# Kernel optimization log

Hardware: AMD Instinct MI355X
Metric: run time of the kernel (lower is better)

Reference implementation:

```python
import jax, jax.numpy as jnp
import numpy as np

NEG_BIG = -9e15  # matches torch's -9000000000000000.0 masked-fill value
ALPHA = 0.2      # LeakyReLU negative slope


def setup_inputs() -> dict:
    key = jax.random.key(0)
    k1, k2, k3, k4 = jax.random.split(key, 4)
    N, F_in, F_out = 8192, 128, 64
    h = jax.random.normal(k1, (N, F_in), dtype=jnp.float32)
    adj = jax.random.randint(k2, (N, N), 0, 2).astype(jnp.float32)
    # Glorot(gain=1.414)-scale params
    W = jax.random.normal(k3, (F_in, F_out), dtype=jnp.float32) * (1.414 * np.sqrt(2.0 / (F_in + F_out)))
    a = jax.random.normal(k4, (2 * F_out, 1), dtype=jnp.float32) * (1.414 * np.sqrt(2.0 / (2 * F_out + 1)))
    return {"h": h, "adj": adj, "W": W, "a": a}


def reference(h, adj, W, a):
    F_out = W.shape[1]
    Wh = h @ W                               # [N, F_out]
    Wh1 = Wh @ a[:F_out, :]                  # [N, 1]
    Wh2 = Wh @ a[F_out:, :]                  # [N, 1]
    e = jax.nn.leaky_relu(Wh1 + Wh2.T, negative_slope=ALPHA)  # [N, N]
    attention = jnp.where(adj > 0, e, NEG_BIG)
    attention = jax.nn.softmax(attention, axis=1)
    # dropout omitted (eval mode / p applied only in training)
    h_prime = attention @ Wh                 # [N, F_out]
    return jax.nn.elu(h_prime)               # concat=True -> ELU
```

## Files before the change

### kernel.cpp

```cpp
#include <hip/hip_runtime.h>
#include <hip/hip_bf16.h>

#define N 8192
#define FIN 128
#define FOUT 64
#define ALPHA 0.2f
#define LOG2E 1.44269504f
#define JSPLIT 4
#define JSPAN (N / JSPLIT)
#define STJ 256
#define NST (JSPAN / STJ)

typedef __attribute__((ext_vector_type(8))) short short8;
typedef __attribute__((ext_vector_type(4))) float f32x4;

static __device__ __forceinline__ unsigned fkey(float x) {
    unsigned u = __float_as_uint(x);
    return (u >> 31) ? ~u : (u | 0x80000000u);
}
static __device__ __forceinline__ float fdecode(unsigned k) {
    unsigned u = (k & 0x80000000u) ? (k & 0x7FFFFFFFu) : ~k;
    return __uint_as_float(u);
}
static __device__ __forceinline__ void gll16(const float* g, float* l) {
    __builtin_amdgcn_global_load_lds(
        (const __attribute__((address_space(1))) unsigned int*)g,
        (__attribute__((address_space(3))) unsigned int*)l, 16, 0, 0);
}

__global__ __launch_bounds__(256) void k_prep(const float* __restrict__ h,
                                              const float* __restrict__ W,
                                              const float* __restrict__ a,
                                              float* __restrict__ Wh,
                                              float* __restrict__ s2,
                                              float* __restrict__ t2,
                                              unsigned* __restrict__ keys) {
    __shared__ float lH[16 * FIN];
    __shared__ float lW[FIN * FOUT];
    __shared__ float red[8];
    const int tid = threadIdx.x;
    const int r0 = blockIdx.x * 16;
    {
        const float4* src = (const float4*)(h + (size_t)r0 * FIN);
        float4* dst = (float4*)lH;
        for (int i = tid; i < 16 * FIN / 4; i += 256) dst[i] = src[i];
        const float4* ws_ = (const float4*)W;
        float4* dw = (float4*)lW;
        for (int i = tid; i < FIN * FOUT / 4; i += 256) dw[i] = ws_[i];
    }
    __syncthreads();
    const int wave = tid >> 6, lane = tid & 63;
    float acc[4] = {0.f, 0.f, 0.f, 0.f};
    for (int k = 0; k < FIN; ++k) {
        float wv = lW[k * FOUT + lane];
#pragma unroll
        for (int r = 0; r < 4; ++r)
            acc[r] = fmaf(lH[(wave * 4 + r) * FIN + k], wv, acc[r]);
    }
    const float a1 = a[lane], a2 = a[FOUT + lane];
    float smx = -1e30f, tmx = -1e30f;
#pragma unroll
    for (int r = 0; r < 4; ++r) {
        int row = r0 + wave * 4 + r;
        Wh[(size_t)row * FOUT + lane] = acc[r];
        float sv = acc[r] * a1, tv = acc[r] * a2;
#pragma unroll
        for (int off = 32; off; off >>= 1) {
            sv += __shfl_xor(sv, off);
            tv += __shfl_xor(tv, off);
        }
        sv *= LOG2E; tv *= LOG2E;
        if (lane == 0) { s2[row] = sv; t2[row] = tv; }
        smx = fmaxf(smx, sv);
        tmx = fmaxf(tmx, tv);
    }
    if (lane == 0) { red[wave] = smx; red[4 + wave] = tmx; }
    __syncthreads();
    if (tid == 0) {
        float ms = fmaxf(fmaxf(red[0], red[1]), fmaxf(red[2], red[3]));
        float mt = fmaxf(fmaxf(red[4], red[5]), fmaxf(red[6], red[7]));
        atomicMax(keys + 0, fkey(ms));
        atomicMax(keys + 1, fkey(mt));
    }
}

__global__ __launch_bounds__(256) void k_pack(const float* __restrict__ Wh,
                                              __hip_bfloat16* __restrict__ WhB) {
    const int c = blockIdx.x;
    const int tn = threadIdx.x >> 6;
    const int lane = threadIdx.x & 63;
    const int quad = lane >> 4, l16 = lane & 15;
    const float* src = Wh + ((size_t)(c * 32 + quad * 8)) * FOUT + tn * 16 + l16;
    union { unsigned short u[8]; short8 v; } frag;
#pragma unroll
    for (int e = 0; e < 8; ++e) {
        __hip_bfloat16 b = __float2bfloat16(src[(size_t)e * FOUT]);
        frag.u[e] = *(unsigned short*)&b;
    }
    *(short8*)&WhB[(((size_t)c * 4 + tn) * 64 + lane) * 8] = frag.v;
}

__global__ __launch_bounds__(256) void k_attn(const float* __restrict__ adj,
                                              const __hip_bfloat16* __restrict__ WhB,
                                              const float* __restrict__ s2,
                                              const float* __restrict__ t2,
                                              const unsigned* __restrict__ keys,
                                              float* __restrict__ acc_ws,
                                              float* __restrict__ l_ws) {
    __shared__ float bufA[2][8 * 512];
    __shared__ float tl[JSPAN];
    const int wave = threadIdx.x >> 6, lane = threadIdx.x & 63;
    const int quad = lane >> 4, l16 = lane & 15;
    const int i0 = blockIdx.x * 16;
    const int jb = blockIdx.y * JSPAN;
    const int u0 = 2 * wave;

    {
        const float4* src = (const float4*)(t2 + jb);
        float4* dst = (float4*)tl;
        for (int i = threadIdx.x; i < JSPAN / 4; i += 256) dst[i] = src[i];
    }
    const float* gaw = adj + (size_t)(i0 + l16) * N + jb + quad * 8;
    gll16(gaw + u0 * 32,      &bufA[0][u0 * 512]);
    gll16(gaw + u0 * 32 + 4,  &bufA[0][u0 * 512 + 256]);
    gll16(gaw + u0 * 32 + 32, &bufA[0][(u0 + 1) * 512]);
    gll16(gaw + u0 * 32 + 36, &bufA[0][(u0 + 1) * 512 + 256]);

    const float mraw = fdecode(keys[0]) + fdecode(keys[1]);
    const float mm = mraw > 0.f ? mraw : ALPHA * mraw;
    const float sm = s2[i0 + l16];
    const short8* BF = (const short8*)WhB;

    f32x4 acc0 = {0,0,0,0}, acc1 = {0,0,0,0}, acc2 = {0,0,0,0}, acc3 = {0,0,0,0};
    float lsum = 0.f;
    __syncthreads();

    for (int st = 0; st < NST; ++st) {
        const int b = st & 1;
        const size_t kc = (size_t)(blockIdx.y * (JSPAN / 32) + st * 8 + u0) * 4;
        short8 B00 = BF[(kc + 0) * 64 + lane];
        short8 B01 = BF[(kc + 1) * 64 + lane];
        short8 B02 = BF[(kc + 2) * 64 + lane];
        short8 B03 = BF[(kc + 3) * 64 + lane];
        short8 B10 = BF[(kc + 4) * 64 + lane];
        short8 B11 = BF[(kc + 5) * 64 + lane];
        short8 B12 = BF[(kc + 6) * 64 + lane];
        short8 B13 = BF[(kc + 7) * 64 + lane];
        __builtin_amdgcn_sched_barrier(0);
        if (st + 1 < NST) {
            const float* g = gaw + (st + 1) * STJ + u0 * 32;
            float* d = &bufA[b ^ 1][u0 * 512];
            gll16(g, d);
            gll16(g + 4, d + 256);
            gll16(g + 32, d + 512);
            gll16(g + 36, d + 768);
        }
        __builtin_amdgcn_sched_barrier(0);
#pragma unroll
        for (int uu = 0; uu < 2; ++uu) {
            const int ul = u0 + uu;
            const float* Au = &bufA[b][ul * 512];
            float4 alo = *(const float4*)(Au + lane * 4);
            float4 ahi = *(const float4*)(Au + 256 + lane * 4);
            const float* Tp = tl + st * STJ + ul * 32 + quad * 8;
            float4 tlo = *(const float4*)Tp;
            float4 thi = *(const float4*)(Tp + 4);
            union { __hip_bfloat162 h2[4]; short8 v; } af;
#pragma unroll
            for (int pp = 0; pp < 4; ++pp) {
                float a0 = (pp < 2) ? ((const float*)&alo)[2 * pp]     : ((const float*)&ahi)[2 * pp - 4];
                float a1 = (pp < 2) ? ((const float*)&alo)[2 * pp + 1] : ((const float*)&ahi)[2 * pp - 3];
                float t0 = (pp < 2) ? ((const float*)&tlo)[2 * pp]     : ((const float*)&thi)[2 * pp - 4];
                float t1 = (pp < 2) ? ((const float*)&tlo)[2 * pp + 1] : ((const float*)&thi)[2 * pp - 3];
                float x0 = sm + t0,                x1 = sm + t1;
                float le0 = fmaxf(x0, ALPHA * x0), le1 = fmaxf(x1, ALPHA * x1);
                float p0 = a0 * exp2f(le0 - mm),   p1 = a1 * exp2f(le1 - mm);
                __hip_bfloat162 pb = __float22bfloat162_rn(make_float2(p0, p1));
                af.h2[pp] = pb;
                lsum += __bfloat162float(pb.x) + __bfloat162float(pb.y);
            }
            if (uu == 0) {
                acc0 = __builtin_amdgcn_mfma_f32_16x16x32_bf16(af.v, B00, acc0, 0, 0, 0);
                acc1 = __builtin_amdgcn_mfma_f32_16x16x32_bf16(af.v, B01, acc1, 0, 0, 0);
                acc2 = __builtin_amdgcn_mfma_f32_16x16x32_bf16(af.v, B02, acc2, 0, 0, 0);
                acc3 = __builtin_amdgcn_mfma_f32_16x16x32_bf16(af.v, B03, acc3, 0, 0, 0);
            } else {
                acc0 = __builtin_amdgcn_mfma_f32_16x16x32_bf16(af.v, B10, acc0, 0, 0, 0);
                acc1 = __builtin_amdgcn_mfma_f32_16x16x32_bf16(af.v, B11, acc1, 0, 0, 0);
                acc2 = __builtin_amdgcn_mfma_f32_16x16x32_bf16(af.v, B12, acc2, 0, 0, 0);
                acc3 = __builtin_amdgcn_mfma_f32_16x16x32_bf16(af.v, B13, acc3, 0, 0, 0);
            }
        }
        __syncthreads();
    }

    lsum += __shfl_xor(lsum, 16);
    lsum += __shfl_xor(lsum, 32);

    float* accr = &bufA[0][0];
    float* shlp = tl;
    *(f32x4*)&accr[((wave * 4 + 0) * 64 + lane) * 4] = acc0;
    *(f32x4*)&accr[((wave * 4 + 1) * 64 + lane) * 4] = acc1;
    *(f32x4*)&accr[((wave * 4 + 2) * 64 + lane) * 4] = acc2;
    *(f32x4*)&accr[((wave * 4 + 3) * 64 + lane) * 4] = acc3;
    if (lane < 16) shlp[wave * 16 + lane] = lsum;
    __syncthreads();

    const int tile = wave;
    f32x4 tot = {0, 0, 0, 0};
#pragma unroll
    for (int w = 0; w < 4; ++w) {
        f32x4 c = *(const f32x4*)&accr[((w * 4 + tile) * 64 + lane) * 4];
        tot[0] += c[0]; tot[1] += c[1]; tot[2] += c[2]; tot[3] += c[3];
    }
#pragma unroll
    for (int r = 0; r < 4; ++r) {
        int row = quad * 4 + r;
        atomicAdd(&acc_ws[(size_t)(i0 + row) * FOUT + tile * 16 + l16], tot[r]);
    }
    if (wave == 0 && lane < 16) {
        float lv = shlp[lane] + shlp[16 + lane] + shlp[32 + lane] + shlp[48 + lane];
        atomicAdd(&l_ws[i0 + lane], lv);
    }
}

__global__ __launch_bounds__(256) void k_final(const float* __restrict__ acc_ws,
                                               const float* __restrict__ l_ws,
                                               float* __restrict__ out) {
    const int idx = blockIdx.x * 256 + threadIdx.x;
    const int row = idx >> 4;
    const float inv = 1.0f / l_ws[row];
    float4 a = ((const float4*)acc_ws)[idx];
    float4 o;
#pragma unroll
    for (int r = 0; r < 4; ++r) {
        float v = ((const float*)&a)[r] * inv;
        ((float*)&o)[r] = v > 0.f ? v : (exp2f(v * LOG2E) - 1.f);
    }
    ((float4*)out)[idx] = o;
}

extern "C" void kernel_launch(void* const* d_in, const int* in_sizes, int n_in,
                              void* d_out, int out_size, void* d_ws, size_t ws_size,
                              hipStream_t stream) {
    const float* h   = (const float*)d_in[0];
    const float* adj = (const float*)d_in[1];
    const float* W   = (const float*)d_in[2];
    const float* a   = (const float*)d_in[3];
    float* out = (float*)d_out;

    char* base = (char*)d_ws;
    float* Wh = (float*)base;                        base += (size_t)N * FOUT * 4;
    __hip_bfloat16* WhB = (__hip_bfloat16*)base;     base += (size_t)N * FOUT * 2;
    float* s2 = (float*)base;                        base += (size_t)N * 4;
    float* t2 = (float*)base;                        base += (size_t)N * 4 + 1024;
    float* acc_ws = (float*)base;                    base += (size_t)N * FOUT * 4;
    float* l_ws = (float*)base;                      base += (size_t)N * 4;
    unsigned* keys = (unsigned*)base;

    hipMemsetAsync(acc_ws, 0, ((size_t)N * FOUT + N) * 4 + 2 * sizeof(unsigned), stream);
    k_prep<<<N / 16, 256, 0, stream>>>(h, W, a, Wh, s2, t2, keys);
    k_pack<<<N / 32, 256, 0, stream>>>(Wh, WhB);
    dim3 ag(N / 16, JSPLIT);
    k_attn<<<ag, 256, 0, stream>>>(adj, WhB, s2, t2, keys, acc_ws, l_ws);
    k_final<<<N * FOUT / 4 / 256, 256, 0, stream>>>(acc_ws, l_ws, out);
}
```

Baseline: 399.1 us.

## Restructure attention tile loads into row-contiguous, padded LDS with triple-stage prefetch

Each wave now loads four full adj rows with fully coalesced 16-byte-per-lane loads into padded LDS rows, instead of scattered 32-byte fragments. It computes the masked exponentials row-wise, writes bf16 probabilities to a separate padded LDS buffer, and reads them back in MFMA fragment layout. Prefetch now runs two stages ahead using manual waitcnt and raw s_barrier, and the row sums are reduced per row with shuffles. This targets better global-load coalescing and deeper memory latency hiding, at the cost of an extra LDS round trip and two barriers per stage. The reuse of buffer b for stage st+2 while other waves may still be reading it relies on the first barrier for ordering. The vmcnt handling inside the loop looks thin.

After: 407.6 us. 1.02x slower.

```diff
diff --git a/kernel.cpp b/kernel.cpp
--- a/kernel.cpp
+++ b/kernel.cpp
@@ -10,6 +10,8 @@
 #define JSPAN (N / JSPLIT)
 #define STJ 256
 #define NST (JSPAN / STJ)
+#define RSA 260
+#define RSP 264
 
 typedef __attribute__((ext_vector_type(8))) short short8;
 typedef __attribute__((ext_vector_type(4))) float f32x4;
@@ -107,37 +109,49 @@
                                               const unsigned* __restrict__ keys,
                                               float* __restrict__ acc_ws,
                                               float* __restrict__ l_ws) {
-    __shared__ float bufA[2][8 * 512];
+    __shared__ float bufA[2][16 * RSA];
+    __shared__ __hip_bfloat16 pbuf[16 * RSP];
     __shared__ float tl[JSPAN];
     const int wave = threadIdx.x >> 6, lane = threadIdx.x & 63;
     const int quad = lane >> 4, l16 = lane & 15;
     const int i0 = blockIdx.x * 16;
     const int jb = blockIdx.y * JSPAN;
-    const int u0 = 2 * wave;
-
-    {
-        const float4* src = (const float4*)(t2 + jb);
-        float4* dst = (float4*)tl;
-        for (int i = threadIdx.x; i < JSPAN / 4; i += 256) dst[i] = src[i];
-    }
-    const float* gaw = adj + (size_t)(i0 + l16) * N + jb + quad * 8;
-    gll16(gaw + u0 * 32,      &bufA[0][u0 * 512]);
-    gll16(gaw + u0 * 32 + 4,  &bufA[0][u0 * 512 + 256]);
-    gll16(gaw + u0 * 32 + 32, &bufA[0][(u0 + 1) * 512]);
-    gll16(gaw + u0 * 32 + 36, &bufA[0][(u0 + 1) * 512 + 256]);
+    const int r0 = 4 * wave;
+
+    for (int i = threadIdx.x; i < JSPAN / 4; i += 256)
+        ((float4*)tl)[i] = ((const float4*)(t2 + jb))[i];
+    asm volatile("s_waitcnt lgkmcnt(0)" ::: "memory");
+    __builtin_amdgcn_sched_barrier(0);
+
+    const float* g0 = adj + (size_t)(i0 + r0 + 0) * N + jb + lane * 4;
+    const float* g1 = g0 + N;
+    const float* g2 = g0 + 2 * N;
+    const float* g3 = g0 + 3 * N;
+
+    gll16(g0, &bufA[0][(r0 + 0) * RSA]);
+    gll16(g1, &bufA[0][(r0 + 1) * RSA]);
+    gll16(g2, &bufA[0][(r0 + 2) * RSA]);
+    gll16(g3, &bufA[0][(r0 + 3) * RSA]);
+    gll16(g0 + STJ, &bufA[1][(r0 + 0) * RSA]);
+    gll16(g1 + STJ, &bufA[1][(r0 + 1) * RSA]);
+    gll16(g2 + STJ, &bufA[1][(r0 + 2) * RSA]);
+    gll16(g3 + STJ, &bufA[1][(r0 + 3) * RSA]);
+    __builtin_amdgcn_sched_barrier(0);
+    asm volatile("s_waitcnt vmcnt(4)" ::: "memory");
 
     const float mraw = fdecode(keys[0]) + fdecode(keys[1]);
     const float mm = mraw > 0.f ? mraw : ALPHA * mraw;
-    const float sm = s2[i0 + l16];
+    float sr[4];
+#pragma unroll
+    for (int rr = 0; rr < 4; ++rr) sr[rr] = s2[i0 + r0 + rr];
     const short8* BF = (const short8*)WhB;
 
     f32x4 acc0 = {0,0,0,0}, acc1 = {0,0,0,0}, acc2 = {0,0,0,0}, acc3 = {0,0,0,0};
-    float lsum = 0.f;
-    __syncthreads();
+    float ls[4] = {0.f, 0.f, 0.f, 0.f};
 
     for (int st = 0; st < NST; ++st) {
         const int b = st & 1;
-        const size_t kc = (size_t)(blockIdx.y * (JSPAN / 32) + st * 8 + u0) * 4;
+        const size_t kc = ((size_t)blockIdx.y * (JSPAN / 32) + st * 8 + 2 * wave) * 4;
         short8 B00 = BF[(kc + 0) * 64 + lane];
         short8 B01 = BF[(kc + 1) * 64 + lane];
         short8 B02 = BF[(kc + 2) * 64 + lane];
@@ -147,65 +161,68 @@
         short8 B12 = BF[(kc + 6) * 64 + lane];
         short8 B13 = BF[(kc + 7) * 64 + lane];
         __builtin_amdgcn_sched_barrier(0);
-        if (st + 1 < NST) {
-            const float* g = gaw + (st + 1) * STJ + u0 * 32;
-            float* d = &bufA[b ^ 1][u0 * 512];
-            gll16(g, d);
-            gll16(g + 4, d + 256);
-            gll16(g + 32, d + 512);
-            gll16(g + 36, d + 768);
+        asm volatile("s_barrier" ::: "memory");
+        float4 tv = *(const float4*)&tl[st * STJ + lane * 4];
+#pragma unroll
+        for (int rr = 0; rr < 4; ++rr) {
+            float4 av = *(const float4*)&bufA[b][(r0 + rr) * RSA + lane * 4];
+            union { __hip_bfloat162 h2[2]; uint2 u2; } pk;
+            float lacc = 0.f;
+#pragma unroll
+            for (int pp = 0; pp < 2; ++pp) {
+                float x0 = sr[rr] + ((const float*)&tv)[2 * pp];
+                float x1 = sr[rr] + ((const float*)&tv)[2 * pp + 1];
+                float le0 = fmaxf(x0, ALPHA * x0), le1 = fmaxf(x1, ALPHA * x1);
+                float p0 = ((const float*)&av)[2 * pp] * exp2f(le0 - mm);
+                float p1 = ((const float*)&av)[2 * pp + 1] * exp2f(le1 - mm);
+                __hip_bfloat162 pb = __float22bfloat162_rn(make_float2(p0, p1));
+                pk.h2[pp] = pb;
+                lacc += __bfloat162float(pb.x) + __bfloat162float(pb.y);
+            }
+            *(uint2*)&pbuf[(r0 + rr) * RSP + lane * 4] = pk.u2;
+            ls[rr] += lacc;
         }
         __builtin_amdgcn_sched_barrier(0);
+        const int sd = (st + 2 < NST ? st + 2 : NST - 1) * STJ;
+        gll16(g0 + sd, &bufA[b][(r0 + 0) * RSA]);
+        gll16(g1 + sd, &bufA[b][(r0 + 1) * RSA]);
+        gll16(g2 + sd, &bufA[b][(r0 + 2) * RSA]);
+        gll16(g3 + sd, &bufA[b][(r0 + 3) * RSA]);
+        __builtin_amdgcn_sched_barrier(0);
+        asm volatile("s_waitcnt lgkmcnt(0)" ::: "memory");
+        asm volatile("s_barrier" ::: "memory");
 #pragma unroll
         for (int uu = 0; uu < 2; ++uu) {
-            const int ul = u0 + uu;
-            const float* Au = &bufA[b][ul * 512];
-            float4 alo = *(const float4*)(Au + lane * 4);
-            float4 ahi = *(const float4*)(Au + 256 + lane * 4);
-            const float* Tp = tl + st * STJ + ul * 32 + quad * 8;
-            float4 tlo = *(const float4*)Tp;
-            float4 thi = *(const float4*)(Tp + 4);
-            union { __hip_bfloat162 h2[4]; short8 v; } af;
-#pragma unroll
-            for (int pp = 0; pp < 4; ++pp) {
-                float a0 = (pp < 2) ? ((const float*)&alo)[2 * pp]     : ((const float*)&ahi)[2 * pp - 4];
-                float a1 = (pp < 2) ? ((const float*)&alo)[2 * pp + 1] : ((const float*)&ahi)[2 * pp - 3];
-                float t0 = (pp < 2) ? ((const float*)&tlo)[2 * pp]     : ((const float*)&thi)[2 * pp - 4];
-                float t1 = (pp < 2) ? ((const float*)&tlo)[2 * pp + 1] : ((const float*)&thi)[2 * pp - 3];
-                float x0 = sm + t0,                x1 = sm + t1;
-                float le0 = fmaxf(x0, ALPHA * x0), le1 = fmaxf(x1, ALPHA * x1);
-                float p0 = a0 * exp2f(le0 - mm),   p1 = a1 * exp2f(le1 - mm);
-                __hip_bfloat162 pb = __float22bfloat162_rn(make_float2(p0, p1));
-                af.h2[pp] = pb;
-                lsum += __bfloat162float(pb.x) + __bfloat162float(pb.y);
-            }
+            short8 af = *(const short8*)&pbuf[l16 * RSP + (2 * wave + uu) * 32 + quad * 8];
             if (uu == 0) {
-                acc0 = __builtin_amdgcn_mfma_f32_16x16x32_bf16(af.v, B00, acc0, 0, 0, 0);
-                acc1 = __builtin_amdgcn_mfma_f32_16x16x32_bf16(af.v, B01, acc1, 0, 0, 0);
-                acc2 = __builtin_amdgcn_mfma_f32_16x16x32_bf16(af.v, B02, acc2, 0, 0, 0);
-                acc3 = __builtin_amdgcn_mfma_f32_16x16x32_bf16(af.v, B03, acc3, 0, 0, 0);
+                acc0 = __builtin_amdgcn_mfma_f32_16x16x32_bf16(af, B00, acc0, 0, 0, 0);
+                acc1 = __builtin_amdgcn_mfma_f32_16x16x32_bf16(af, B01, acc1, 0, 0, 0);
+                acc2 = __builtin_amdgcn_mfma_f32_16x16x32_bf16(af, B02, acc2, 0, 0, 0);
+                acc3 = __builtin_amdgcn_mfma_f32_16x16x32_bf16(af, B03, acc3, 0, 0, 0);
             } else {
-                acc0 = __builtin_amdgcn_mfma_f32_16x16x32_bf16(af.v, B10, acc0, 0, 0, 0);
-                acc1 = __builtin_amdgcn_mfma_f32_16x16x32_bf16(af.v, B11, acc1, 0, 0, 0);
-                acc2 = __builtin_amdgcn_mfma_f32_16x16x32_bf16(af.v, B12, acc2, 0, 0, 0);
-                acc3 = __builtin_amdgcn_mfma_f32_16x16x32_bf16(af.v, B13, acc3, 0, 0, 0);
+                acc0 = __builtin_amdgcn_mfma_f32_16x16x32_bf16(af, B10, acc0, 0, 0, 0);
+                acc1 = __builtin_amdgcn_mfma_f32_16x16x32_bf16(af, B11, acc1, 0, 0, 0);
+                acc2 = __builtin_amdgcn_mfma_f32_16x16x32_bf16(af, B12, acc2, 0, 0, 0);
+                acc3 = __builtin_amdgcn_mfma_f32_16x16x32_bf16(af, B13, acc3, 0, 0, 0);
             }
         }
-        __syncthreads();
-    }
-
-    lsum += __shfl_xor(lsum, 16);
-    lsum += __shfl_xor(lsum, 32);
+    }
+    __syncthreads();
+
+#pragma unroll
+    for (int rr = 0; rr < 4; ++rr) {
+        float v = ls[rr];
+#pragma unroll
+        for (int off = 32; off; off >>= 1) v += __shfl_xor(v, off);
+        if (lane == 0) atomicAdd(&l_ws[i0 + r0 + rr], v);
+    }
 
     float* accr = &bufA[0][0];
-    float* shlp = tl;
     *(f32x4*)&accr[((wave * 4 + 0) * 64 + lane) * 4] = acc0;
     *(f32x4*)&accr[((wave * 4 + 1) * 64 + lane) * 4] = acc1;
     *(f32x4*)&accr[((wave * 4 + 2) * 64 + lane) * 4] = acc2;
     *(f32x4*)&accr[((wave * 4 + 3) * 64 + lane) * 4] = acc3;
-    if (lane < 16) shlp[wave * 16 + lane] = lsum;
-    __syncthreads();
-
+    __syncthreads();
     const int tile = wave;
     f32x4 tot = {0, 0, 0, 0};
 #pragma unroll
@@ -217,10 +234,6 @@
     for (int r = 0; r < 4; ++r) {
         int row = quad * 4 + r;
         atomicAdd(&acc_ws[(size_t)(i0 + row) * FOUT + tile * 16 + l16], tot[r]);
-    }
-    if (wave == 0 && lane < 16) {
-        float lv = shlp[lane] + shlp[16 + lane] + shlp[32 + lane] + shlp[48 + lane];
-        atomicAdd(&l_ws[i0 + lane], lv);
     }
 }
 
```
